# Kernel tuning notes

Hardware: AMD Instinct MI355X
Metric: run time of the kernel (lower is better)

Reference implementation:

```python
import jax, jax.numpy as jnp
import numpy as np
from jax import lax

FH, FW = 38, 63          # feature map H,W (600x1000 image, stride 16)
A = 9                    # anchors per location (3 scales x 3 ratios)
POOL = 7                 # cfg.POOLING_SIZE
PRE_NMS, POST_NMS = 6000, 300
NMS_THRESH = 0.7
IM_H, IM_W = 600.0, 1000.0
STRIDE = 16.0


def _make_anchors(h, w, stride=16):
    ratios = np.array([0.5, 1.0, 2.0]); scales = np.array([8.0, 16.0, 32.0])
    base = 16.0; ctr = (base - 1.0) / 2.0
    ws = np.round(np.sqrt(base * base / ratios)); hs = np.round(ws * ratios)
    ws = (ws[:, None] * scales[None, :]).ravel(); hs = (hs[:, None] * scales[None, :]).ravel()
    ba = np.stack([ctr - 0.5 * (ws - 1), ctr - 0.5 * (hs - 1),
                   ctr + 0.5 * (ws - 1), ctr + 0.5 * (hs - 1)], 1)
    sx, sy = np.meshgrid(np.arange(w) * stride, np.arange(h) * stride)
    shifts = np.stack([sx.ravel(), sy.ravel(), sx.ravel(), sy.ravel()], 1)
    return (shifts[:, None, :] + ba[None]).reshape(-1, 4).astype(np.float32)


def _conv(x, w, b, pad):
    y = lax.conv_general_dilated(x, w, (1, 1), pad,
                                 dimension_numbers=('NCHW', 'OIHW', 'NCHW'))
    return y + b[None, :, None, None]


def _bbox_transform_inv(anchors, deltas):
    w = anchors[:, 2] - anchors[:, 0] + 1.0
    h = anchors[:, 3] - anchors[:, 1] + 1.0
    cx = anchors[:, 0] + 0.5 * w
    cy = anchors[:, 1] + 0.5 * h
    dx, dy, dw, dh = deltas[:, 0], deltas[:, 1], deltas[:, 2], deltas[:, 3]
    pcx = dx * w + cx; pcy = dy * h + cy
    pw = jnp.exp(dw) * w; ph = jnp.exp(dh) * h
    return jnp.stack([pcx - 0.5 * pw, pcy - 0.5 * ph,
                      pcx + 0.5 * pw, pcy + 0.5 * ph], 1)


def _nms_keep(boxes, thresh):
    # greedy NMS over score-sorted boxes, fixed-size keep mask
    x1, y1, x2, y2 = boxes[:, 0], boxes[:, 1], boxes[:, 2], boxes[:, 3]
    areas = (x2 - x1 + 1.0) * (y2 - y1 + 1.0)
    iw = jnp.maximum(jnp.minimum(x2[:, None], x2[None, :])
                     - jnp.maximum(x1[:, None], x1[None, :]) + 1.0, 0.0)
    ih = jnp.maximum(jnp.minimum(y2[:, None], y2[None, :])
                     - jnp.maximum(y1[:, None], y1[None, :]) + 1.0, 0.0)
    inter = iw * ih
    iou = inter / (areas[:, None] + areas[None, :] - inter)
    n = boxes.shape[0]; ar = jnp.arange(n)
    def body(i, keep):
        sup = (iou[i] > thresh) & (ar > i) & keep[i]
        return keep & ~sup
    return lax.fori_loop(0, n, body, jnp.ones((n,), bool))


def _crop_and_resize(feat, boxes, crop):
    # feat [C,H,W]; boxes [R,4] normalized (y1,x1,y2,x2); TF crop_and_resize semantics
    C, H, W = feat.shape
    t = jnp.arange(crop, dtype=feat.dtype) / (crop - 1)
    def one(box):
        by1, bx1, by2, bx2 = box
        ys = by1 * (H - 1) + t * (by2 - by1) * (H - 1)
        xs = bx1 * (W - 1) + t * (bx2 - bx1) * (W - 1)
        y0f = jnp.floor(ys); x0f = jnp.floor(xs)
        wy = (ys - y0f)[None, :, None]; wx = (xs - x0f)[None, None, :]
        y0 = jnp.clip(y0f, 0, H - 1).astype(jnp.int32)
        y1i = jnp.clip(y0f + 1, 0, H - 1).astype(jnp.int32)
        x0 = jnp.clip(x0f, 0, W - 1).astype(jnp.int32)
        x1i = jnp.clip(x0f + 1, 0, W - 1).astype(jnp.int32)
        f00 = feat[:, y0][:, :, x0]; f01 = feat[:, y0][:, :, x1i]
        f10 = feat[:, y1i][:, :, x0]; f11 = feat[:, y1i][:, :, x1i]
        return (f00 * (1 - wy) * (1 - wx) + f01 * (1 - wy) * wx
                + f10 * wy * (1 - wx) + f11 * wy * wx)
    return jax.vmap(one)(boxes)


def _forward(net_conv, w_rpn, b_rpn, w_cls, b_cls, w_bbox, b_bbox, anchors):
    # _region_proposal: 3x3 rpn conv + relu, 1x1 cls / bbox heads
    rpn = jax.nn.relu(_conv(net_conv, w_rpn, b_rpn, 'SAME'))
    cls = _conv(rpn, w_cls, b_cls, 'VALID')    # [1,2A,H,W]
    bbox = _conv(rpn, w_bbox, b_bbox, 'VALID')  # [1,4A,H,W]
    # view(1,2,-1,W) softmax: channel a pairs with channel a+A (bg/fg)
    bg, fg = cls[:, :A], cls[:, A:]
    fg_prob = jax.nn.softmax(jnp.stack([bg, fg], axis=1), axis=1)[:, 1]  # [1,A,H,W]
    scores = jnp.transpose(fg_prob, (0, 2, 3, 1)).reshape(-1)            # (H*W*A,)
    deltas = jnp.transpose(bbox, (0, 2, 3, 1)).reshape(-1, 4)
    proposals = _bbox_transform_inv(anchors, deltas)
    proposals = jnp.stack([jnp.clip(proposals[:, 0], 0.0, IM_W - 1.0),
                           jnp.clip(proposals[:, 1], 0.0, IM_H - 1.0),
                           jnp.clip(proposals[:, 2], 0.0, IM_W - 1.0),
                           jnp.clip(proposals[:, 3], 0.0, IM_H - 1.0)], 1)
    # proposal selection is non-differentiable (rois.detach() in original)
    scores_sg = lax.stop_gradient(scores)
    props_sg = lax.stop_gradient(proposals)
    _, order = lax.top_k(scores_sg, PRE_NMS)
    boxes = props_sg[order]
    keep = _nms_keep(boxes, NMS_THRESH)
    idx = jnp.sort(jnp.where(keep, jnp.arange(PRE_NMS), PRE_NMS))[:POST_NMS]
    rois = boxes[jnp.minimum(idx, PRE_NMS - 1)]  # [300,4] (x1,y1,x2,y2)
    # _crop_pool_layer with max_pool=True: crop to 14x14 then 2x2 max pool
    H, W = net_conv.shape[2], net_conv.shape[3]
    x1 = rois[:, 0] / STRIDE; y1 = rois[:, 1] / STRIDE
    x2 = rois[:, 2] / STRIDE; y2 = rois[:, 3] / STRIDE
    norm = jnp.stack([y1 / (H - 1), x1 / (W - 1), y2 / (H - 1), x2 / (W - 1)], 1)
    crops = _crop_and_resize(net_conv[0], norm, 2 * POOL)  # [300,C,14,14]
    R, C = crops.shape[0], crops.shape[1]
    return crops.reshape(R, C, POOL, 2, POOL, 2).max(axis=(3, 5))  # [300,C,7,7]


def setup_inputs():
    key = jax.random.key(0)
    ks = jax.random.split(key, 4)
    net_conv = jax.random.normal(ks[0], (1, 512, FH, FW), jnp.float32)
    w_rpn = jax.random.normal(ks[1], (512, 512, 3, 3), jnp.float32) * 0.01
    b_rpn = jnp.zeros((512,), jnp.float32)
    w_cls = jax.random.normal(ks[2], (2 * A, 512, 1, 1), jnp.float32) * 0.01
    b_cls = jnp.zeros((2 * A,), jnp.float32)
    w_bbox = jax.random.normal(ks[3], (4 * A, 512, 1, 1), jnp.float32) * 0.01
    b_bbox = jnp.zeros((4 * A,), jnp.float32)
    anchors = jnp.asarray(_make_anchors(FH, FW))
    return {"net_conv": net_conv, "w_rpn": w_rpn, "b_rpn": b_rpn,
            "w_cls": w_cls, "b_cls": b_cls, "w_bbox": w_bbox,
            "b_bbox": b_bbox, "anchors": anchors}


def reference(net_conv, w_rpn, b_rpn, w_cls, b_cls, w_bbox, b_bbox, anchors):
    return _forward(net_conv, w_rpn, b_rpn, w_cls, b_cls, w_bbox, b_bbox, anchors)
```

## Files before the change

kernel.cpp:

```cpp
#include <hip/hip_runtime.h>
#include <stdint.h>

#define NPOS 2394
#define CIN 512
#define KK 4608
#define NANCH 21546
#define PRE 6000
#define POST 300
#define NWORD 94
#define NQ 8
#define QLEN 2694
#define FEATT_BYTES 4902912

#define OFF_BH    0
#define OFF_BL    4718592
#define OFF_FPH   9437184
#define OFF_FPL   12166144
#define OFF_P0    14895104
#define OFF_P1    19798016
#define OFF_P2    24700928
#define OFF_KEYS  0
#define OFF_PROP  180224
#define OFF_RPART 532480
#define OFF_SBOX  1228800
#define OFF_DIAG  1335296
#define OFF_MASK  4718592

#define NBORDER 138752

typedef _Float16 half8 __attribute__((ext_vector_type(8)));
typedef float f32x4 __attribute__((ext_vector_type(4)));

__device__ __forceinline__ void gload16(const void* g, void* l) {
    __builtin_amdgcn_global_load_lds((const __attribute__((address_space(1))) void*)g,
                                     (__attribute__((address_space(3))) void*)l, 16, 0, 0);
}

__device__ __forceinline__ unsigned long long rl64(unsigned long long v, int l) {
    union { unsigned long long q; unsigned int d[2]; } s; s.q = v;
    unsigned int lo = __builtin_amdgcn_readlane(s.d[0], l);
    unsigned int hi = __builtin_amdgcn_readlane(s.d[1], l);
    return ((unsigned long long)hi << 32) | (unsigned long long)lo;
}

__global__ __launch_bounds__(256) void k_prep_all(const float* __restrict__ in,
                                                  const float* __restrict__ w,
                                                  float* __restrict__ featT,
                                                  _Float16* __restrict__ FPH,
                                                  _Float16* __restrict__ FPL,
                                                  _Float16* __restrict__ BH,
                                                  _Float16* __restrict__ BL) {
    int blk = blockIdx.x;
    if (blk < 1200) {
        __shared__ float tl[32][33];
        int tx = threadIdx.x & 31, tg = threadIdx.x >> 5;
        int posBase = (blk % 75) * 32, ciBase = (blk / 75) * 32;
#pragma unroll
        for (int j = 0; j < 4; ++j) {
            int ci = ciBase + tg + j * 8;
            int pos = posBase + tx;
            tl[tg + j * 8][tx] = (pos < NPOS) ? in[(size_t)ci * NPOS + pos] : 0.f;
        }
        __syncthreads();
#pragma unroll
        for (int j = 0; j < 4; ++j) {
            int pos = posBase + tg + j * 8;
            int ci = ciBase + tx;
            if (pos < NPOS) {
                float v = tl[tx][tg + j * 8];
                featT[(size_t)pos * 512 + ci] = v;
                int h = pos / 63, wq = pos - h * 63;
                int o = ((h + 1) * 65 + (wq + 1)) * 512 + ci;
                float a = v * 16.f;
                _Float16 ah = (_Float16)a;
                FPH[o] = ah;
                FPL[o] = (_Float16)(a - (float)ah);
            }
        }
        return;
    }
    int b = blk - 1200;
    if (b >= 9216) {
        int i2 = (b - 9216) * 256 + threadIdx.x;
        if (i2 < NBORDER) {
            int bi = i2 >> 9, ci = i2 & 511;
            int hp, wp;
            if (bi < 195) {
                hp = (bi < 65) ? 0 : ((bi < 130) ? 39 : 40);
                wp = (bi < 65) ? bi : ((bi < 130) ? bi - 65 : bi - 130);
            } else {
                int j = bi - 195;
                hp = 1 + (j >> 1);
                wp = (j & 1) ? 64 : 0;
            }
            int o = (hp * 65 + wp) * 512 + ci;
            FPH[o] = (_Float16)0.f; FPL[o] = (_Float16)0.f;
        }
        return;
    }
    int idx = b * 256 + threadIdx.x;
    int co = idx / KK;
    int rem = idx - co * KK;
    int p = rem >> 9;
    int ci = rem & 511;
    float bv = w[(co * CIN + ci) * 9 + p] * 128.f;
    _Float16 bh = (_Float16)bv;
    _Float16 bl = (_Float16)(bv - (float)bh);
    BH[idx] = bh; BL[idx] = bl;
}

__global__ __launch_bounds__(256, 3) void k_conv3_mfma(
    const _Float16* __restrict__ FPH, const _Float16* __restrict__ FPL,
    const _Float16* __restrict__ BHp, const _Float16* __restrict__ BLp,
    float* __restrict__ P0, float* __restrict__ P1, float* __restrict__ P2)
{
    __shared__ __align__(16) char lds[49152];
    const int t = threadIdx.x;
    const int wave = t >> 6, lane = t & 63;

    const int bid = blockIdx.x;
    const int swz = (bid & 7) * 57 + (bid >> 3);
    const int z = swz / 152;
    const int rem = swz - z * 152;
    const int coB = rem / 19;
    const int posB = rem - coB * 19;
    const int posBase = posB * 128;
    const int coBase  = coB * 64;
    float* __restrict__ P = (z == 0) ? P0 : ((z == 1) ? P1 : P2);

    const int wm = wave >> 1, wn = wave & 1;
    const int lr = lane & 15, lg = lane >> 4;

    int addrA[4][2], addrB[2][2];
#pragma unroll
    for (int m = 0; m < 4; ++m) {
        int row = wm * 64 + m * 16 + lr;
        int x = row & 7;
        addrA[m][0] = row * 128 + ((lg ^ x) << 4);
        addrA[m][1] = row * 128 + (((4 + lg) ^ x) << 4);
    }
#pragma unroll
    for (int n = 0; n < 2; ++n) {
        int row = wn * 32 + n * 16 + lr;
        int x = row & 7;
        addrB[n][0] = 32768 + row * 128 + ((lg ^ x) << 4);
        addrB[n][1] = 32768 + row * 128 + (((4 + lg) ^ x) << 4);
    }

    int baseA[4], ldsAo[4];
#pragma unroll
    for (int s = 0; s < 4; ++s) {
        int row = (wave * 4 + s) * 8 + (lane >> 3);
        int pos = posBase + row;
        int h = pos / 63;
        int w = pos - h * 63;
        int swzb = ((lane & 7) ^ (row & 7)) * 8;
        baseA[s] = (h * 65 + w) * 512 + swzb;
        ldsAo[s] = (wave * 4 + s) * 1024 + lane * 16;
    }
    int baseB[2], ldsBo[2];
#pragma unroll
    for (int s = 0; s < 2; ++s) {
        int row = (wave * 2 + s) * 8 + (lane >> 3);
        int swzb = ((lane & 7) ^ (row & 7)) * 8;
        baseB[s] = (coBase + row) * KK + swzb;
        ldsBo[s] = 32768 + (wave * 2 + s) * 1024 + lane * 16;
    }

    f32x4 acc[4][2];
#pragma unroll
    for (int m = 0; m < 4; ++m)
#pragma unroll
        for (int n = 0; n < 2; ++n) acc[m][n] = (f32x4){0.f, 0.f, 0.f, 0.f};

    const int kbeg = z * 1536;
    for (int step = 0; step < 24; ++step) {
        int k0 = kbeg + step * 64;
        int p = k0 >> 9;
        int ci0 = k0 & 511;
        int kh = p / 3;
        int kw = p - kh * 3;
        int dA = (kh * 65 + kw) * 512 + ci0;
#pragma unroll
        for (int s = 0; s < 4; ++s) {
            int so = baseA[s] + dA;
            gload16(FPH + so, lds + ldsAo[s]);
            gload16(FPL + so, lds + 16384 + ldsAo[s]);
        }
#pragma unroll
        for (int s = 0; s < 2; ++s) {
            int so = baseB[s] + k0;
            gload16(BHp + so, lds + ldsBo[s]);
            gload16(BLp + so, lds + 8192 + ldsBo[s]);
        }
        __syncthreads();
#pragma unroll
        for (int ks = 0; ks < 2; ++ks) {
            half8 aH[4], aL[4], bH[2], bL[2];
#pragma unroll
            for (int m = 0; m < 4; ++m) {
                aH[m] = *(const half8*)(lds + addrA[m][ks]);
                aL[m] = *(const half8*)(lds + 16384 + addrA[m][ks]);
            }
#pragma unroll
            for (int n = 0; n < 2; ++n) {
                bH[n] = *(const half8*)(lds + addrB[n][ks]);
                bL[n] = *(const half8*)(lds + 8192 + addrB[n][ks]);
            }
#pragma unroll
            for (int m = 0; m < 4; ++m)
#pragma unroll
                for (int n = 0; n < 2; ++n) {
                    acc[m][n] = __builtin_amdgcn_mfma_f32_16x16x32_f16(aH[m], bH[n], acc[m][n], 0, 0, 0);
                    acc[m][n] = __builtin_amdgcn_mfma_f32_16x16x32_f16(aH[m], bL[n], acc[m][n], 0, 0, 0);
                    acc[m][n] = __builtin_amdgcn_mfma_f32_16x16x32_f16(aL[m], bH[n], acc[m][n], 0, 0, 0);
                }
        }
        __syncthreads();
    }

#pragma unroll
    for (int m = 0; m < 4; ++m) {
        int pbase = posBase + wm * 64 + m * 16 + lg * 4;
        int co = coBase + wn * 32 + lr;
#pragma unroll
        for (int r = 0; r < 4; ++r) {
            int pos = pbase + r;
            if (pos < NPOS) {
                P[(size_t)pos * 512 + co]      = acc[m][0][r] * (1.f / 2048.f);
                P[(size_t)pos * 512 + co + 16] = acc[m][1][r] * (1.f / 2048.f);
            }
        }
    }
}

__global__ __launch_bounds__(256) void k_heads(const float* __restrict__ P0,
                                               const float* __restrict__ P1,
                                               const float* __restrict__ P2,
                                               const float* __restrict__ brpn,
                                               const float* __restrict__ wcls,
                                               const float* __restrict__ bcls,
                                               const float* __restrict__ wbbox,
                                               const float* __restrict__ bbbox,
                                               const float* __restrict__ anchors,
                                               float* __restrict__ proposals,
                                               unsigned long long* __restrict__ keys) {
    __shared__ float x[512];
    __shared__ float part[54][4];
    __shared__ float logit[54];
    int pos = blockIdx.x;
    int t = threadIdx.x;
    {
        size_t o = (size_t)pos * 512 + t;
        float v0 = P0[o] + P1[o] + P2[o] + brpn[t];
        float v1 = P0[o + 256] + P1[o + 256] + P2[o + 256] + brpn[t + 256];
        x[t] = v0 > 0.f ? v0 : 0.f;
        x[t + 256] = v1 > 0.f ? v1 : 0.f;
    }
    __syncthreads();
    if (t < 216) {
        int o = t >> 2, q = t & 3;
        const float* wr = (o < 18) ? (wcls + o * 512) : (wbbox + (o - 18) * 512);
        float s = 0.f;
        int base = q * 128;
#pragma unroll 4
        for (int k2 = 0; k2 < 128; ++k2) s += x[base + k2] * wr[base + k2];
        part[o][q] = s;
    }
    __syncthreads();
    if (t < 54) {
        float b = (t < 18) ? bcls[t] : bbbox[t - 18];
        logit[t] = part[t][0] + part[t][1] + part[t][2] + part[t][3] + b;
    }
    __syncthreads();
    if (t < 9) {
        int a = t;
        float bg = logit[a], fg = logit[9 + a];
        float score = 1.f / (1.f + expf(bg - fg));
        float dx = logit[18 + 4 * a], dy = logit[19 + 4 * a];
        float dw = logit[20 + 4 * a], dh = logit[21 + 4 * a];
        int idx = pos * 9 + a;
        float ax1 = anchors[idx * 4 + 0], ay1 = anchors[idx * 4 + 1];
        float ax2 = anchors[idx * 4 + 2], ay2 = anchors[idx * 4 + 3];
        float aw = ax2 - ax1 + 1.f, ah = ay2 - ay1 + 1.f;
        float cx = ax1 + 0.5f * aw, cy = ay1 + 0.5f * ah;
        float pcx = dx * aw + cx, pcy = dy * ah + cy;
        float pw = expf(dw) * aw, ph = expf(dh) * ah;
        float x1 = fminf(fmaxf(pcx - 0.5f * pw, 0.f), 999.f);
        float y1 = fminf(fmaxf(pcy - 0.5f * ph, 0.f), 599.f);
        float x2 = fminf(fmaxf(pcx + 0.5f * pw, 0.f), 999.f);
        float y2 = fminf(fmaxf(pcy + 0.5f * ph, 0.f), 599.f);
        proposals[idx * 4 + 0] = x1; proposals[idx * 4 + 1] = y1;
        proposals[idx * 4 + 2] = x2; proposals[idx * 4 + 3] = y2;
        union { float f; unsigned int i; } sv; sv.f = score;
        keys[idx] = (((unsigned long long)sv.i) << 32) |
                    (unsigned long long)(0xFFFFFFFFu - (unsigned)idx);
    }
}

__global__ __launch_bounds__(256) void k_rank_partial(const unsigned long long* __restrict__ keys,
                                                      unsigned int* __restrict__ rpart) {
    __shared__ unsigned long long kc[1024];
    int i = blockIdx.x * 256 + threadIdx.x;
    int q = blockIdx.y;
    unsigned long long myk = (i < NANCH) ? keys[i] : 0xFFFFFFFFFFFFFFFFull;
    int j0 = q * QLEN;
    int j1 = j0 + QLEN; if (j1 > NANCH) j1 = NANCH;
    unsigned int cnt = 0;
    for (int base = j0; base < j1; base += 1024) {
        int nload = j1 - base; if (nload > 1024) nload = 1024;
        __syncthreads();
        for (int u = threadIdx.x; u < 1024; u += 256)
            kc[u] = (base + u < j1) ? keys[base + u] : 0ull;
        __syncthreads();
        for (int u = 0; u < nload; ++u)
            cnt += (kc[u] > myk) ? 1u : 0u;
    }
    if (i < NANCH) rpart[i * NQ + q] = cnt;
}

__global__ void k_rank_scatter(const unsigned int* __restrict__ rpart,
                               const float* __restrict__ proposals,
                               float* __restrict__ sboxes) {
    int i = blockIdx.x * 256 + threadIdx.x;
    if (i >= NANCH) return;
    unsigned int r = 0;
#pragma unroll
    for (int q = 0; q < NQ; q++) r += rpart[i * NQ + q];
    if (r < PRE) {
        sboxes[r * 4 + 0] = proposals[i * 4 + 0];
        sboxes[r * 4 + 1] = proposals[i * 4 + 1];
        sboxes[r * 4 + 2] = proposals[i * 4 + 2];
        sboxes[r * 4 + 3] = proposals[i * 4 + 3];
    }
}

__global__ __launch_bounds__(64) void k_nms_mask(const float* __restrict__ sboxes,
                                                 unsigned long long* __restrict__ mask,
                                                 unsigned long long* __restrict__ diag4) {
    __shared__ float bx[64][5];
    int ib = blockIdx.x, jb = blockIdx.y;
    int lane = threadIdx.x;
    int j = jb * 64 + lane;
    if (j < PRE) {
        bx[lane][0] = sboxes[j * 4 + 0]; bx[lane][1] = sboxes[j * 4 + 1];
        bx[lane][2] = sboxes[j * 4 + 2]; bx[lane][3] = sboxes[j * 4 + 3];
    } else {
        bx[lane][0] = 3e8f; bx[lane][1] = 3e8f; bx[lane][2] = 3e8f; bx[lane][3] = 3e8f;
    }
    __syncthreads();
    int i = ib * 64 + lane;
    if (i >= PRE) return;
    float x1 = sboxes[i * 4 + 0], y1 = sboxes[i * 4 + 1];
    float x2 = sboxes[i * 4 + 2], y2 = sboxes[i * 4 + 3];
    float ar = (x2 - x1 + 1.f) * (y2 - y1 + 1.f);
    unsigned long long bits = 0;
#pragma unroll 4
    for (int u = 0; u < 64; u++) {
        int j2 = jb * 64 + u;
        float iw = fminf(x2, bx[u][2]) - fmaxf(x1, bx[u][0]) + 1.f;
        float ih = fminf(y2, bx[u][3]) - fmaxf(y1, bx[u][1]) + 1.f;
        iw = fmaxf(iw, 0.f); ih = fmaxf(ih, 0.f);
        float inter = iw * ih;
        float arj = (bx[u][2] - bx[u][0] + 1.f) * (bx[u][3] - bx[u][1] + 1.f);
        float iou = inter / (ar + arj - inter);
        if (iou > 0.7f && j2 > i) bits |= (1ull << u);
    }
    mask[(size_t)i * NWORD + jb] = bits;
    if ((jb >> 2) == (ib >> 2)) diag4[(size_t)i * 4 + (jb & 3)] = bits;
}

#define NSB 24
#define SBW 256
#define NSLOT 20
__global__ __launch_bounds__(64) void k_nms_scan(const unsigned long long* __restrict__ mask,
                                                 const unsigned long long* __restrict__ diag4,
                                                 const float* __restrict__ sboxes,
                                                 float* __restrict__ outF) {
    __shared__ __align__(16) unsigned long long tile[2][SBW * 4];
    __shared__ __align__(16) char ldsrow[NSLOT * 1024];
    __shared__ int ldsk[POST];
    const int lane = threadIdx.x;
    const char* dg = (const char*)diag4;

    for (int c = 0; c < 8; ++c)
        gload16(dg + c * 1024 + (size_t)lane * 16, (char*)tile[0] + c * 1024);

    unsigned long long rem0 = 0, rem1 = 0;
    int nk = 0, npend = 0;

    for (int sb = 0; sb < NSB; ++sb) {
        if (sb + 1 < NSB) {
            const char* src = dg + (size_t)(sb + 1) * 8192;
            char* dst = (char*)tile[(sb + 1) & 1];
            for (int c = 0; c < 8; ++c)
                gload16(src + c * 1024 + (size_t)lane * 16, dst + c * 1024);
            asm volatile("s_waitcnt vmcnt(8)" ::: "memory");
        } else {
            asm volatile("s_waitcnt vmcnt(0)" ::: "memory");
        }
        __builtin_amdgcn_sched_barrier(0);

        for (int q = 0; q < npend; ++q) {
            const unsigned long long* lr = (const unsigned long long*)(ldsrow + q * 1024);
            rem0 |= lr[lane];
            if (lane < NWORD - 64) rem1 |= lr[64 + lane];
        }
        npend = 0;

        const unsigned long long* tl = tile[sb & 1];
        unsigned long long d[4][4];
#pragma unroll
        for (int q = 0; q < 4; ++q) {
            ulonglong2 e0 = *(const ulonglong2*)&tl[(q * 64 + lane) * 4];
            ulonglong2 e1 = *(const ulonglong2*)&tl[(q * 64 + lane) * 4 + 2];
            d[q][0] = e0.x; d[q][1] = e0.y; d[q][2] = e1.x; d[q][3] = e1.y;
        }

        const int w0 = 4 * sb;
        const int base = sb * SBW;
        unsigned long long rmw[4];
#pragma unroll
        for (int j = 0; j < 4; ++j) {
            int w = w0 + j;
            rmw[j] = (w < 64) ? rl64(rem0, w) : ((w < NWORD) ? rl64(rem1, w - 64) : ~0ull);
        }

#pragma unroll
        for (int p = 0; p < 4; ++p) {
            int w = w0 + p;
            if (w >= NWORD) break;
            const unsigned long long valid = (w == NWORD - 1) ? ((1ull << 48) - 1) : ~0ull;
            unsigned long long above = ~0ull;
            unsigned long long keptm = 0;
            for (;;) {
                unsigned long long a = ~rmw[p] & valid & above;
                if (!a) break;
                int u = (int)(__ffsll((long long)a) - 1);
                keptm |= 1ull << u;
                ++nk;
                if (nk == POST) break;
                rmw[p] |= rl64(d[p][p], u);
                above = (u == 63) ? 0ull : (~0ull << (u + 1));
            }
            {
                unsigned long long bits = keptm;
                while (bits) {
                    int u = (int)(__ffsll((long long)bits) - 1); bits &= bits - 1;
#pragma unroll
                    for (int j = p + 1; j < 4; ++j) rmw[j] |= rl64(d[p][j], u);
                }
            }
            unsigned long long bits = keptm;
            int nkb = nk - __builtin_popcountll(keptm);
            while (bits) {
                int u = (int)(__ffsll((long long)bits) - 1); bits &= bits - 1;
                int i = base + p * 64 + u;
                if (lane == 0) ldsk[nkb] = i;
                ++nkb;
                if (npend == NSLOT) {
                    asm volatile("s_waitcnt vmcnt(0)" ::: "memory");
                    __builtin_amdgcn_sched_barrier(0);
                    for (int q = 0; q < NSLOT; ++q) {
                        const unsigned long long* lr = (const unsigned long long*)(ldsrow + q * 1024);
                        rem0 |= lr[lane];
                        if (lane < NWORD - 64) rem1 |= lr[64 + lane];
                    }
                    npend = 0;
                }
                gload16((const char*)(mask + (size_t)i * NWORD) + (size_t)lane * 16,
                        ldsrow + npend * 1024);
                ++npend;
            }
            if (nk >= POST) goto done;
        }
    }
done:
    asm volatile("s_waitcnt vmcnt(0)" ::: "memory");
    float4 bx[5];
#pragma unroll
    for (int i = 0; i < 5; ++i) {
        int r = lane + i * 64;
        if (r < POST) {
            int ki = (r < nk) ? ldsk[r] : PRE - 1;
            bx[i] = *reinterpret_cast<const float4*>(sboxes + ki * 4);
        }
    }
    asm volatile("s_waitcnt vmcnt(0)" ::: "memory");
    __builtin_amdgcn_sched_barrier(0);
#pragma unroll
    for (int i = 0; i < 5; ++i) {
        int r = lane + i * 64;
        if (r < POST) {
#pragma unroll
            for (int cg = 0; cg < 8; ++cg)
                *reinterpret_cast<float4*>(outF + (size_t)(r * 512 + cg * 64) * 49) = bx[i];
        }
    }
}

__global__ __launch_bounds__(256) void k_crop_fast(const float* __restrict__ featT,
                                                   float* out) {
    __shared__ float lds[4][49 * 65];
    int r = blockIdx.x;
    int w = threadIdx.x >> 6, lane = threadIdx.x & 63;
    int cg = blockIdx.y * 4 + w;
    int c = cg * 64 + lane;
    float* chunk = out + (size_t)(r * 512 + cg * 64) * 49;
    const float4 b = *reinterpret_cast<const float4*>(chunk);
    float x1 = b.x, y1 = b.y, x2 = b.z, y2 = b.w;
    float by1 = (y1 / 16.f) / 37.f, bx1 = (x1 / 16.f) / 62.f;
    float by2 = (y2 / 16.f) / 37.f, bx2 = (x2 / 16.f) / 62.f;
    float dyn = by2 - by1, dxn = bx2 - bx1;
    for (int e = 0; e < 49; ++e) {
        int oy = e / 7, ox = e - oy * 7;
        float vv[4];
#pragma unroll
        for (int dy = 0; dy < 2; ++dy) {
            int sy = 2 * oy + dy;
            float ty = (float)sy / 13.f;
            float ys = by1 * 37.f + (ty * dyn) * 37.f;
            float yf = floorf(ys);
            float wy = ys - yf;
            int y0  = (int)fminf(fmaxf(yf, 0.f), 37.f);
            int y1i = (int)fminf(fmaxf(yf + 1.f, 0.f), 37.f);
#pragma unroll
            for (int dxx = 0; dxx < 2; ++dxx) {
                int sx = 2 * ox + dxx;
                float tx = (float)sx / 13.f;
                float xs = bx1 * 62.f + (tx * dxn) * 62.f;
                float xf = floorf(xs);
                float wx = xs - xf;
                int x0  = (int)fminf(fmaxf(xf, 0.f), 62.f);
                int x1i = (int)fminf(fmaxf(xf + 1.f, 0.f), 62.f);
                float f00 = featT[(size_t)(y0 * 63 + x0) * 512 + c];
                float f01 = featT[(size_t)(y0 * 63 + x1i) * 512 + c];
                float f10 = featT[(size_t)(y1i * 63 + x0) * 512 + c];
                float f11 = featT[(size_t)(y1i * 63 + x1i) * 512 + c];
                vv[dy * 2 + dxx] = f00 * (1.f - wy) * (1.f - wx) + f01 * (1.f - wy) * wx +
                                   f10 * wy * (1.f - wx) + f11 * wy * wx;
            }
        }
        lds[w][e * 65 + lane] = fmaxf(fmaxf(vv[0], vv[1]), fmaxf(vv[2], vv[3]));
    }
    __syncthreads();
    for (int i = lane; i < 64 * 49; i += 64) {
        int cl = i / 49, e = i - cl * 49;
        chunk[i] = lds[w][e * 65 + cl];
    }
}

__global__ __launch_bounds__(64) void k_crop_slow(const float* __restrict__ net,
                                                  float* out) {
    int r = blockIdx.x, cg = blockIdx.y;
    int lane = threadIdx.x;
    int c = cg * 64 + lane;
    const float4 b = *reinterpret_cast<const float4*>(out + (size_t)(r * 512 + cg * 64) * 49);
    float x1 = b.x, y1 = b.y, x2 = b.z, y2 = b.w;
    float by1 = (y1 / 16.f) / 37.f, bx1 = (x1 / 16.f) / 62.f;
    float by2 = (y2 / 16.f) / 37.f, bx2 = (x2 / 16.f) / 62.f;
    float dyn = by2 - by1, dxn = bx2 - bx1;
    const float* fc = net + (size_t)c * NPOS;
    float* orow = out + ((size_t)r * 512 + c) * 49;
    for (int e = 0; e < 49; ++e) {
        int oy = e / 7, ox = e - oy * 7;
        float vv[4];
#pragma unroll
        for (int dy = 0; dy < 2; ++dy) {
            int sy = 2 * oy + dy;
            float ty = (float)sy / 13.f;
            float ys = by1 * 37.f + (ty * dyn) * 37.f;
            float yf = floorf(ys);
            float wy = ys - yf;
            int y0  = (int)fminf(fmaxf(yf, 0.f), 37.f);
            int y1i = (int)fminf(fmaxf(yf + 1.f, 0.f), 37.f);
#pragma unroll
            for (int dxx = 0; dxx < 2; ++dxx) {
                int sx = 2 * ox + dxx;
                float tx = (float)sx / 13.f;
                float xs = bx1 * 62.f + (tx * dxn) * 62.f;
                float xf = floorf(xs);
                float wx = xs - xf;
                int x0  = (int)fminf(fmaxf(xf, 0.f), 62.f);
                int x1i = (int)fminf(fmaxf(xf + 1.f, 0.f), 62.f);
                float f00 = fc[y0 * 63 + x0];
                float f01 = fc[y0 * 63 + x1i];
                float f10 = fc[y1i * 63 + x0];
                float f11 = fc[y1i * 63 + x1i];
                vv[dy * 2 + dxx] = f00 * (1.f - wy) * (1.f - wx) + f01 * (1.f - wy) * wx +
                                   f10 * wy * (1.f - wx) + f11 * wy * wx;
            }
        }
        orow[e] = fmaxf(fmaxf(vv[0], vv[1]), fmaxf(vv[2], vv[3]));
    }
}

extern "C" void kernel_launch(void* const* d_in, const int* in_sizes, int n_in,
                              void* d_out, int out_size, void* d_ws, size_t ws_size,
                              hipStream_t stream) {
    auto find = [&](int count, int fallback) {
        for (int i = 0; i < n_in; ++i) if (in_sizes[i] == count) return i;
        return fallback;
    };
    const float* net   = (const float*)d_in[find(NPOS * CIN, 0)];
    const float* wrpn  = (const float*)d_in[find(512 * KK, 1)];
    const float* brpn  = (const float*)d_in[find(512, 2)];
    const float* wcls  = (const float*)d_in[find(18 * 512, 3)];
    const float* bcls  = (const float*)d_in[find(18, 4)];
    const float* wbbox = (const float*)d_in[find(36 * 512, 5)];
    const float* bbbox = (const float*)d_in[find(36, 6)];
    const float* anch  = (const float*)d_in[find(NANCH * 4, 7)];

    char* ob = (char*)d_out;
    _Float16* BH             = (_Float16*)(ob + OFF_BH);
    _Float16* BL             = (_Float16*)(ob + OFF_BL);
    _Float16* FPH            = (_Float16*)(ob + OFF_FPH);
    _Float16* FPL            = (_Float16*)(ob + OFF_FPL);
    float* P0                = (float*)(ob + OFF_P0);
    float* P1                = (float*)(ob + OFF_P1);
    float* P2                = (float*)(ob + OFF_P2);
    unsigned long long* keys = (unsigned long long*)(ob + OFF_KEYS);
    float* proposals         = (float*)(ob + OFF_PROP);
    unsigned int* rpart      = (unsigned int*)(ob + OFF_RPART);
    float* sboxes            = (float*)(ob + OFF_SBOX);
    unsigned long long* diag4= (unsigned long long*)(ob + OFF_DIAG);
    unsigned long long* mask = (unsigned long long*)(ob + OFF_MASK);
    float* outF              = (float*)d_out;

    const bool ws_ok = (ws_size >= (size_t)FEATT_BYTES);
    float* featT = ws_ok ? (float*)d_ws : (float*)(ob + OFF_P0);

    hipLaunchKernelGGL(k_prep_all, dim3(1200 + 9216 + 543), dim3(256), 0, stream,
                       net, wrpn, featT, FPH, FPL, BH, BL);
    hipLaunchKernelGGL(k_conv3_mfma, dim3(456), dim3(256), 0, stream, FPH, FPL, BH, BL, P0, P1, P2);
    hipLaunchKernelGGL(k_heads, dim3(NPOS), dim3(256), 0, stream, P0, P1, P2, brpn, wcls, bcls, wbbox, bbbox, anch, proposals, keys);
    hipLaunchKernelGGL(k_rank_partial, dim3(85, NQ), dim3(256), 0, stream, keys, rpart);
    hipLaunchKernelGGL(k_rank_scatter, dim3(85), dim3(256), 0, stream, rpart, proposals, sboxes);
    hipLaunchKernelGGL(k_nms_mask, dim3(NWORD, NWORD), dim3(64), 0, stream, sboxes, mask, diag4);
    hipLaunchKernelGGL(k_nms_scan, dim3(1), dim3(64), 0, stream, mask, diag4, sboxes, outF);
    if (ws_ok)
        hipLaunchKernelGGL(k_crop_fast, dim3(POST, 2), dim3(256), 0, stream, featT, outF);
    else
        hipLaunchKernelGGL(k_crop_slow, dim3(POST, 8), dim3(64), 0, stream, net, outF);
}
```

Before: 380.9 us.

## Defer suppression-row merges one superblock via diag8 lookahead and double-buffered row slots

The NMS mask kernel now stores an 8-word diagonal band (current plus next superblock) instead of 4. The single-wave scan uses it to apply the next superblock's suppression directly from the tile, so it can defer merging the full mask rows it fetched for one superblock. Row fetches go into two alternating slot groups and are padded with dummy loads so a fixed vmcnt wait covers them. This hides global-load latency of mask rows behind a superblock's scan, at the cost of more LDS, a larger diagonal array and extra dummy loads.

New measurement: 403.7 us. 1.06x slower.

```diff
diff --git a/kernel.cpp b/kernel.cpp
--- a/kernel.cpp
+++ b/kernel.cpp
@@ -337,7 +337,7 @@
 
 __global__ __launch_bounds__(64) void k_nms_mask(const float* __restrict__ sboxes,
                                                  unsigned long long* __restrict__ mask,
-                                                 unsigned long long* __restrict__ diag4) {
+                                                 unsigned long long* __restrict__ diag8) {
     __shared__ float bx[64][5];
     int ib = blockIdx.x, jb = blockIdx.y;
     int lane = threadIdx.x;
@@ -367,54 +367,64 @@
         if (iou > 0.7f && j2 > i) bits |= (1ull << u);
     }
     mask[(size_t)i * NWORD + jb] = bits;
-    if ((jb >> 2) == (ib >> 2)) diag4[(size_t)i * 4 + (jb & 3)] = bits;
+    int rel = jb - ((ib >> 2) << 2);
+    if ((unsigned)rel < 8u) diag8[(size_t)i * 8 + rel] = bits;
 }
 
 #define NSB 24
 #define SBW 256
-#define NSLOT 20
+#define RSLOT 16
 __global__ __launch_bounds__(64) void k_nms_scan(const unsigned long long* __restrict__ mask,
-                                                 const unsigned long long* __restrict__ diag4,
+                                                 const unsigned long long* __restrict__ diag8,
                                                  const float* __restrict__ sboxes,
                                                  float* __restrict__ outF) {
-    __shared__ __align__(16) unsigned long long tile[2][SBW * 4];
-    __shared__ __align__(16) char ldsrow[NSLOT * 1024];
+    __shared__ __align__(16) unsigned long long tile[2][SBW * 8];
+    __shared__ __align__(16) char ldsrow[2][RSLOT][1024];
+    __shared__ __align__(16) char dummyrow[1024];
     __shared__ int ldsk[POST];
     const int lane = threadIdx.x;
-    const char* dg = (const char*)diag4;
-
-    for (int c = 0; c < 8; ++c)
+    const char* dg = (const char*)diag8;
+
+    for (int c = 0; c < 16; ++c)
         gload16(dg + c * 1024 + (size_t)lane * 16, (char*)tile[0] + c * 1024);
+    for (int c = 0; c < 16; ++c)
+        gload16((const char*)mask + (size_t)lane * 16, dummyrow);
 
     unsigned long long rem0 = 0, rem1 = 0;
-    int nk = 0, npend = 0;
+    unsigned long long nxt[4] = {0, 0, 0, 0};
+    int nreal[2] = {0, 0};
+    int nk = 0;
 
     for (int sb = 0; sb < NSB; ++sb) {
         if (sb + 1 < NSB) {
-            const char* src = dg + (size_t)(sb + 1) * 8192;
+            const char* src = dg + (size_t)(sb + 1) * 16384;
             char* dst = (char*)tile[(sb + 1) & 1];
-            for (int c = 0; c < 8; ++c)
+            for (int c = 0; c < 16; ++c)
                 gload16(src + c * 1024 + (size_t)lane * 16, dst + c * 1024);
-            asm volatile("s_waitcnt vmcnt(8)" ::: "memory");
         } else {
-            asm volatile("s_waitcnt vmcnt(0)" ::: "memory");
-        }
+            for (int c = 0; c < 16; ++c)
+                gload16((const char*)mask + (size_t)lane * 16, dummyrow);
+        }
+        asm volatile("s_waitcnt vmcnt(32)" ::: "memory");
         __builtin_amdgcn_sched_barrier(0);
 
-        for (int q = 0; q < npend; ++q) {
-            const unsigned long long* lr = (const unsigned long long*)(ldsrow + q * 1024);
+        const int g = sb & 1;
+        for (int q = 0; q < nreal[g]; ++q) {
+            const unsigned long long* lr = (const unsigned long long*)(ldsrow[g][q]);
             rem0 |= lr[lane];
             if (lane < NWORD - 64) rem1 |= lr[64 + lane];
         }
-        npend = 0;
+        nreal[g] = 0;
 
         const unsigned long long* tl = tile[sb & 1];
-        unsigned long long d[4][4];
+        unsigned long long d[4][8];
 #pragma unroll
         for (int q = 0; q < 4; ++q) {
-            ulonglong2 e0 = *(const ulonglong2*)&tl[(q * 64 + lane) * 4];
-            ulonglong2 e1 = *(const ulonglong2*)&tl[(q * 64 + lane) * 4 + 2];
-            d[q][0] = e0.x; d[q][1] = e0.y; d[q][2] = e1.x; d[q][3] = e1.y;
+#pragma unroll
+            for (int e = 0; e < 4; ++e) {
+                ulonglong2 v = *(const ulonglong2*)&tl[(size_t)(q * 64 + lane) * 8 + e * 2];
+                d[q][e * 2] = v.x; d[q][e * 2 + 1] = v.y;
+            }
         }
 
         const int w0 = 4 * sb;
@@ -423,8 +433,11 @@
 #pragma unroll
         for (int j = 0; j < 4; ++j) {
             int w = w0 + j;
-            rmw[j] = (w < 64) ? rl64(rem0, w) : ((w < NWORD) ? rl64(rem1, w - 64) : ~0ull);
-        }
+            unsigned long long rv = (w < 64) ? rl64(rem0, w)
+                                             : ((w < NWORD) ? rl64(rem1, w - 64) : ~0ull);
+            rmw[j] = rv | nxt[j];
+        }
+        unsigned long long nxtn[4] = {0, 0, 0, 0};
 
 #pragma unroll
         for (int p = 0; p < 4; ++p) {
@@ -449,6 +462,8 @@
                     int u = (int)(__ffsll((long long)bits) - 1); bits &= bits - 1;
 #pragma unroll
                     for (int j = p + 1; j < 4; ++j) rmw[j] |= rl64(d[p][j], u);
+#pragma unroll
+                    for (int j = 4; j < 8; ++j) nxtn[j - 4] |= rl64(d[p][j], u);
                 }
             }
             unsigned long long bits = keptm;
@@ -458,22 +473,28 @@
                 int i = base + p * 64 + u;
                 if (lane == 0) ldsk[nkb] = i;
                 ++nkb;
-                if (npend == NSLOT) {
+                if (nreal[g] == RSLOT) {
                     asm volatile("s_waitcnt vmcnt(0)" ::: "memory");
                     __builtin_amdgcn_sched_barrier(0);
-                    for (int q = 0; q < NSLOT; ++q) {
-                        const unsigned long long* lr = (const unsigned long long*)(ldsrow + q * 1024);
-                        rem0 |= lr[lane];
-                        if (lane < NWORD - 64) rem1 |= lr[64 + lane];
+                    for (int gg = 0; gg < 2; ++gg) {
+                        for (int q = 0; q < nreal[gg]; ++q) {
+                            const unsigned long long* lr = (const unsigned long long*)(ldsrow[gg][q]);
+                            rem0 |= lr[lane];
+                            if (lane < NWORD - 64) rem1 |= lr[64 + lane];
+                        }
+                        nreal[gg] = 0;
                     }
-                    npend = 0;
                 }
                 gload16((const char*)(mask + (size_t)i * NWORD) + (size_t)lane * 16,
-                        ldsrow + npend * 1024);
-                ++npend;
+                        ldsrow[g][nreal[g]]);
+                ++nreal[g];
             }
             if (nk >= POST) goto done;
         }
+        for (int c = nreal[g]; c < RSLOT; ++c)
+            gload16((const char*)mask + (size_t)lane * 16, dummyrow);
+#pragma unroll
+        for (int j = 0; j < 4; ++j) nxt[j] = nxtn[j];
     }
 done:
     asm volatile("s_waitcnt vmcnt(0)" ::: "memory");
@@ -623,7 +644,7 @@
     float* proposals         = (float*)(ob + OFF_PROP);
     unsigned int* rpart      = (unsigned int*)(ob + OFF_RPART);
     float* sboxes            = (float*)(ob + OFF_SBOX);
-    unsigned long long* diag4= (unsigned long long*)(ob + OFF_DIAG);
+    unsigned long long* diag8= (unsigned long long*)(ob + OFF_DIAG);
     unsigned long long* mask = (unsigned long long*)(ob + OFF_MASK);
     float* outF              = (float*)d_out;
 
@@ -636,8 +657,8 @@
     hipLaunchKernelGGL(k_heads, dim3(NPOS), dim3(256), 0, stream, P0, P1, P2, brpn, wcls, bcls, wbbox, bbbox, anch, proposals, keys);
     hipLaunchKernelGGL(k_rank_partial, dim3(85, NQ), dim3(256), 0, stream, keys, rpart);
     hipLaunchKernelGGL(k_rank_scatter, dim3(85), dim3(256), 0, stream, rpart, proposals, sboxes);
-    hipLaunchKernelGGL(k_nms_mask, dim3(NWORD, NWORD), dim3(64), 0, stream, sboxes, mask, diag4);
-    hipLaunchKernelGGL(k_nms_scan, dim3(1), dim3(64), 0, stream, mask, diag4, sboxes, outF);
+    hipLaunchKernelGGL(k_nms_mask, dim3(NWORD, NWORD), dim3(64), 0, stream, sboxes, mask, diag8);
+    hipLaunchKernelGGL(k_nms_scan, dim3(1), dim3(64), 0, stream, mask, diag8, sboxes, outF);
     if (ws_ok)
         hipLaunchKernelGGL(k_crop_fast, dim3(POST, 2), dim3(256), 0, stream, featT, outF);
     else
```
